# Optimization experiments

Hardware: AMD Instinct MI355X
Metric: run time of the kernel (lower is better)

Reference implementation:

```python
import jax, jax.numpy as jnp
import numpy as np

GMAX = 1.0   # args.gmax
GMIN = 0.01  # args.gmin
EPS = 0.1    # args.e_train


def setup_inputs() -> dict:
    key = jax.random.key(0)
    k1, k2, k3, k4 = jax.random.split(key, 4)
    N, B, NIN, NOUT, E = 8, 32, 128, 128, 1024
    # analog signals live in [0, 1]
    a_previous = jax.random.uniform(k1, (N, B, NIN, E), dtype=jnp.float32)
    # conductance params (clamped to [-gmax, gmax] in forward)
    theta = jax.random.uniform(k2, (NIN + 2, NOUT), dtype=jnp.float32) * 2.0 - 1.0
    # per-replica multiplicative noise seed in [0, 1); forward maps to 1 +- eps
    noise = jax.random.uniform(k3, (N, NIN + 2, NOUT), dtype=jnp.float32)
    # printed-tanh activation params eta = [offset, scale, shift, slope]
    eta = jnp.array([0.0, 1.0, 0.0, 1.0], dtype=jnp.float32) + 0.1 * jax.random.normal(k4, (4,), dtype=jnp.float32)
    return {"a_previous": a_previous, "theta": theta, "noise": noise, "eta": eta}


def reference(a_previous, theta, noise, eta):
    sg = jax.lax.stop_gradient
    # theta property: clamp + gmin pruning with straight-through estimator
    t = jnp.clip(theta, -GMAX, GMAX)
    t = jnp.where(jnp.abs(t) < GMIN, 0.0, t)
    theta_eff = sg(t) + theta - sg(theta)
    # theta_noisy: replicate over N with multiplicative uniform noise in [1-eps, 1+eps]
    theta_noisy = theta_eff[None, :, :] * ((noise * 2.0 - 1.0) * EPS + 1.0)  # [N, M, O], M = n_in+2
    # W: abs-normalized conductances per output column group
    abs_tn = jnp.abs(theta_noisy)
    W = abs_tn / (jnp.sum(abs_tn, axis=1, keepdims=True) + 1e-10)
    # sign masks (constants w.r.t. grad: values fully overwritten in torch)
    pos = sg((theta_noisy >= 0.0).astype(theta_noisy.dtype))
    neg = 1.0 - pos
    # a: [N, B, n_in, E] -> [N, B, E, n_in]; append ones and zeros columns
    a_r = jnp.transpose(a_previous, (0, 1, 3, 2))
    ones = jnp.ones(a_r.shape[:3] + (1,), a_r.dtype)
    zeros = jnp.zeros_like(ones)
    a_ext = jnp.concatenate([a_r, ones, zeros], axis=3)  # [N, B, E, M]
    # INV: unipolar complement; zero the last (zeros) column after inversion
    a_neg = (1.0 - a_ext).at[..., -1].set(0.0)
    # split-sign MAC: z [N, B, E, n_out]
    z = (jnp.einsum('nbem,nmo->nbeo', a_ext, W * pos)
         + jnp.einsum('nbem,nmo->nbeo', a_neg, W * neg))
    # printed tanh activation
    act = eta[0] + eta[1] * jnp.tanh((z - eta[2]) * eta[3])
    # back to [N, B, n_out, E]
    return jnp.transpose(act, (0, 1, 3, 2))
```

## Files before the change

### kernel.cpp

```cpp
#include <hip/hip_runtime.h>
#include <hip/hip_bf16.h>
#include <stdint.h>

#define N_REP 8
#define BATCH 32
#define NIN   128
#define NOUT  128
#define EDIM  1024
#define MDIM  130

typedef __attribute__((ext_vector_type(8))) short short8;
typedef __attribute__((ext_vector_type(4))) float f32x4;

__device__ __forceinline__ unsigned short f2bf(float f) {
    union { float f; uint32_t u; } v;
    v.f = f;
    uint32_t u = v.u;
    uint32_t r = u + 0x7fffu + ((u >> 16) & 1u);
    return (unsigned short)(r >> 16);
}

__device__ __forceinline__ uint32_t pk2bf(float lo, float hi) {
    __hip_bfloat162 h = __float22bfloat162_rn(make_float2(lo, hi));
    uint32_t d;
    __builtin_memcpy(&d, &h, 4);
    return d;
}

__global__ __launch_bounds__(64)
void prep_kernel(const float* __restrict__ theta,
                 const float* __restrict__ noise,
                 unsigned short* __restrict__ Sg,
                 float* __restrict__ biasg) {
    const int n = blockIdx.x >> 7;
    const int o = blockIdx.x & 127;
    const int lane = threadIdx.x;

    const float* nb = noise + (size_t)n * MDIM * NOUT + o;
    auto tn_at = [&](int m) -> float {
        float t = theta[m * NOUT + o];
        t = fminf(fmaxf(t, -1.f), 1.f);
        if (fabsf(t) < 0.01f) t = 0.f;
        return t * fmaf(nb[m * NOUT], 0.2f, 0.9f);
    };

    const float t0 = tn_at(lane);
    const float t1 = tn_at(lane + 64);
    const float t2 = (lane < 2) ? tn_at(128 + lane) : 0.f;

    float s = fabsf(t0) + fabsf(t1) + fabsf(t2);
#pragma unroll
    for (int d = 1; d < 64; d <<= 1) s += __shfl_xor(s, d, 64);
    const float inv = 1.f / (s + 1e-10f);

    const float w0 = fabsf(t0) * inv, w1 = fabsf(t1) * inv;
    unsigned short* srow = Sg + ((size_t)n * NOUT + o) * NIN;
    srow[lane]      = f2bf(t0 >= 0.f ? w0 : -w0);
    srow[lane + 64] = f2bf(t1 >= 0.f ? w1 : -w1);

    float b = (t0 < 0.f ? w0 : 0.f) + (t1 < 0.f ? w1 : 0.f);
    if (lane == 0 && t2 >= 0.f) b += fabsf(t2) * inv;
#pragma unroll
    for (int d = 1; d < 64; d <<= 1) b += __shfl_xor(b, d, 64);
    if (lane == 0) biasg[n * NOUT + o] = b;
}

__global__ __launch_bounds__(256, 3)
void gemm_kernel(const float* __restrict__ a,
                 const unsigned short* __restrict__ Sg,
                 const float* __restrict__ biasg,
                 const float* __restrict__ eta,
                 float* __restrict__ out) {
    const int bid  = blockIdx.x;
    const int tid  = threadIdx.x;
    const int lane = tid & 63;
    const int wv   = tid >> 6;
    const int r    = lane & 15;
    const int q    = lane >> 4;
    const int nb   = bid >> 3;
    const int n    = nb >> 5;
    const int e0w  = (((bid & 7) << 2) | wv) << 5;

    const float* abase = a + (size_t)nb * (NIN * EDIM) + e0w + r;

    float e0 = eta[0], e1 = eta[1], e2 = eta[2], e3 = eta[3];
    asm volatile("" : "+v"(e0), "+v"(e1), "+v"(e2), "+v"(e3));

    float bl[8];
#pragma unroll
    for (int fo = 0; fo < 8; ++fo)
        bl[fo] = biasg[n * NOUT + (fo << 4) + r];

    f32x4 acc[8][2];
#pragma unroll
    for (int fo = 0; fo < 8; ++fo)
#pragma unroll
        for (int fe = 0; fe < 2; ++fe)
            acc[fo][fe] = (f32x4){0.f, 0.f, 0.f, 0.f};

    const unsigned short* sbase = Sg + ((size_t)(n * NOUT) << 7) + (q << 3);

#pragma unroll
    for (int ks = 0; ks < 4; ++ks) {
        float av[2][8];
#pragma unroll
        for (int fe = 0; fe < 2; ++fe)
#pragma unroll
            for (int j = 0; j < 8; ++j)
                av[fe][j] = abase[(size_t)((ks << 5) + (q << 3) + j) * EDIM + (fe << 4)];

        short8 sf[8];
#pragma unroll
        for (int fo = 0; fo < 8; ++fo)
            sf[fo] = *(const short8*)(sbase + ((size_t)((fo << 4) + r) << 7) + (ks << 5));

        short8 af[2];
#pragma unroll
        for (int fe = 0; fe < 2; ++fe) {
            uint32_t d[4];
#pragma unroll
            for (int t = 0; t < 4; ++t)
                d[t] = pk2bf(av[fe][2 * t], av[fe][2 * t + 1]);
            __builtin_memcpy(&af[fe], d, 16);
        }

#pragma unroll
        for (int fo = 0; fo < 8; ++fo)
#pragma unroll
            for (int fe = 0; fe < 2; ++fe)
                acc[fo][fe] = __builtin_amdgcn_mfma_f32_16x16x32_bf16(
                    af[fe], sf[fo], acc[fo][fe], 0, 0, 0);
    }

    float* obase = out + (size_t)nb * (NOUT * EDIM) + e0w;
#pragma unroll
    for (int fo = 0; fo < 8; ++fo) {
        float* orow = obase + (size_t)((fo << 4) + r) * EDIM;
        const float bv = bl[fo];
#pragma unroll
        for (int fe = 0; fe < 2; ++fe) {
            f32x4 res;
#pragma unroll
            for (int i = 0; i < 4; ++i) {
                const float z = acc[fo][fe][i] + bv;
                const float y = (z - e2) * e3;
                const float ex = __expf(2.f * y);
                const float th = 1.f - 2.f * __builtin_amdgcn_rcpf(ex + 1.f);
                res[i] = fmaf(e1, th, e0);
            }
            *(f32x4*)(orow + (fe << 4) + (q << 2)) = res;
        }
    }
}

extern "C" void kernel_launch(void* const* d_in, const int* in_sizes, int n_in,
                              void* d_out, int out_size, void* d_ws, size_t ws_size,
                              hipStream_t stream) {
    const float* a     = (const float*)d_in[0];
    const float* theta = (const float*)d_in[1];
    const float* noise = (const float*)d_in[2];
    const float* eta   = (const float*)d_in[3];
    float* out = (float*)d_out;

    unsigned short* Sg = (unsigned short*)d_ws;
    float* biasg = (float*)((char*)d_ws + (size_t)N_REP * NOUT * NIN * sizeof(unsigned short));

    prep_kernel<<<N_REP * NOUT, 64, 0, stream>>>(theta, noise, Sg, biasg);
    gemm_kernel<<<N_REP * BATCH * 8, 256, 0, stream>>>(a, Sg, biasg, eta, out);
}
```

Baseline: 268.6 us.

## Stage A tiles through LDS with float4 loads and register prefetch

Activation loads switch from scalar per-lane global reads to float4 vector loads. The values are packed into bf16 pairs along k and written to a per-wave, padded, double-buffered LDS slice, from which the MFMA A-fragments are read. The next k-slice is prefetched into registers while MFMAs run on the current one, and weight fragments are loaded closer to their use. This aims to cut the number of global memory instructions and overlap load latency with compute, at the cost of LDS traffic and extra registers.

```diff
diff --git a/kernel.cpp b/kernel.cpp
--- a/kernel.cpp
+++ b/kernel.cpp
@@ -8,6 +8,8 @@
 #define NOUT  128
 #define EDIM  1024
 #define MDIM  130
+#define SROW  36
+#define SLICE (16 * SROW)
 
 typedef __attribute__((ext_vector_type(8))) short short8;
 typedef __attribute__((ext_vector_type(4))) float f32x4;
@@ -71,25 +73,46 @@
                  const float* __restrict__ biasg,
                  const float* __restrict__ eta,
                  float* __restrict__ out) {
+    __shared__ uint32_t Alds[4][2][SLICE];
     const int bid  = blockIdx.x;
+    const int nb   = bid >> 3;
+    const int n    = nb >> 5;
+    const int eb   = bid & 7;
     const int tid  = threadIdx.x;
     const int lane = tid & 63;
     const int wv   = tid >> 6;
     const int r    = lane & 15;
     const int q    = lane >> 4;
-    const int nb   = bid >> 3;
-    const int n    = nb >> 5;
-    const int e0w  = (((bid & 7) << 2) | wv) << 5;
+    const int e0   = (eb << 7) + (wv << 5);
 
-    const float* abase = a + (size_t)nb * (NIN * EDIM) + e0w + r;
+    const int mp_l = lane >> 2;
+    const int ec   = (lane & 3) << 2;
+    const float* abase = a + (size_t)nb * (NIN * EDIM) + e0 + ec;
+    uint32_t* L = &Alds[wv][0][0];
 
-    float e0 = eta[0], e1 = eta[1], e2 = eta[2], e3 = eta[3];
-    asm volatile("" : "+v"(e0), "+v"(e1), "+v"(e2), "+v"(e3));
+    float4 va[2], vb[2];
+    auto issue = [&](int t) {
+        const float* gp = abase + (size_t)(2 * mp_l + (t << 5)) * EDIM;
+#pragma unroll
+        for (int i = 0; i < 2; ++i) {
+            va[i] = *(const float4*)(gp + (i << 4));
+            vb[i] = *(const float4*)(gp + EDIM + (i << 4));
+        }
+    };
+    auto pack_write = [&](int buf) {
+#pragma unroll
+        for (int i = 0; i < 2; ++i) {
+            uint4 d;
+            d.x = pk2bf(va[i].x, vb[i].x);
+            d.y = pk2bf(va[i].y, vb[i].y);
+            d.z = pk2bf(va[i].z, vb[i].z);
+            d.w = pk2bf(va[i].w, vb[i].w);
+            *(uint4*)&L[buf * SLICE + mp_l * SROW + ec + (i << 4)] = d;
+        }
+    };
 
-    float bl[8];
-#pragma unroll
-    for (int fo = 0; fo < 8; ++fo)
-        bl[fo] = biasg[n * NOUT + (fo << 4) + r];
+    float e0f = eta[0], e1f = eta[1], e2f = eta[2], e3f = eta[3];
+    asm volatile("" : "+v"(e0f), "+v"(e1f), "+v"(e2f), "+v"(e3f));
 
     f32x4 acc[8][2];
 #pragma unroll
@@ -100,53 +123,55 @@
 
     const unsigned short* sbase = Sg + ((size_t)(n * NOUT) << 7) + (q << 3);
 
+    issue(0);
+    pack_write(0);
+    issue(1);
+
 #pragma unroll
-    for (int ks = 0; ks < 4; ++ks) {
-        float av[2][8];
-#pragma unroll
-        for (int fe = 0; fe < 2; ++fe)
-#pragma unroll
-            for (int j = 0; j < 8; ++j)
-                av[fe][j] = abase[(size_t)((ks << 5) + (q << 3) + j) * EDIM + (fe << 4)];
-
-        short8 sf[8];
-#pragma unroll
-        for (int fo = 0; fo < 8; ++fo)
-            sf[fo] = *(const short8*)(sbase + ((size_t)((fo << 4) + r) << 7) + (ks << 5));
-
+    for (int t = 0; t < 4; ++t) {
+        const int buf = t & 1;
         short8 af[2];
 #pragma unroll
         for (int fe = 0; fe < 2; ++fe) {
             uint32_t d[4];
 #pragma unroll
-            for (int t = 0; t < 4; ++t)
-                d[t] = pk2bf(av[fe][2 * t], av[fe][2 * t + 1]);
+            for (int jj = 0; jj < 4; ++jj)
+                d[jj] = L[buf * SLICE + ((q << 2) + jj) * SROW + (fe << 4) + r];
             __builtin_memcpy(&af[fe], d, 16);
         }
-
 #pragma unroll
-        for (int fo = 0; fo < 8; ++fo)
+        for (int fo2 = 0; fo2 < 4; ++fo2) {
+            const short8 s0 = *(const short8*)(sbase + ((size_t)((fo2 << 5) + r) << 7) + (t << 5));
+            const short8 s1 = *(const short8*)(sbase + ((size_t)((fo2 << 5) + 16 + r) << 7) + (t << 5));
 #pragma unroll
-            for (int fe = 0; fe < 2; ++fe)
-                acc[fo][fe] = __builtin_amdgcn_mfma_f32_16x16x32_bf16(
-                    af[fe], sf[fo], acc[fo][fe], 0, 0, 0);
+            for (int fe = 0; fe < 2; ++fe) {
+                acc[fo2 * 2][fe] = __builtin_amdgcn_mfma_f32_16x16x32_bf16(
+                    af[fe], s0, acc[fo2 * 2][fe], 0, 0, 0);
+                acc[fo2 * 2 + 1][fe] = __builtin_amdgcn_mfma_f32_16x16x32_bf16(
+                    af[fe], s1, acc[fo2 * 2 + 1][fe], 0, 0, 0);
+            }
+        }
+        if (t < 3) {
+            pack_write(buf ^ 1);
+            if (t < 2) issue(t + 2);
+        }
     }
 
-    float* obase = out + (size_t)nb * (NOUT * EDIM) + e0w;
+    float* obase = out + (size_t)nb * (NOUT * EDIM) + e0;
 #pragma unroll
     for (int fo = 0; fo < 8; ++fo) {
+        const float bv = biasg[n * NOUT + (fo << 4) + r];
         float* orow = obase + (size_t)((fo << 4) + r) * EDIM;
-        const float bv = bl[fo];
 #pragma unroll
         for (int fe = 0; fe < 2; ++fe) {
             f32x4 res;
 #pragma unroll
             for (int i = 0; i < 4; ++i) {
                 const float z = acc[fo][fe][i] + bv;
-                const float y = (z - e2) * e3;
+                const float y = (z - e2f) * e3f;
                 const float ex = __expf(2.f * y);
                 const float th = 1.f - 2.f * __builtin_amdgcn_rcpf(ex + 1.f);
-                res[i] = fmaf(e1, th, e0);
+                res[i] = fmaf(e1f, th, e0f);
             }
             *(f32x4*)(orow + (fe << 4) + (q << 2)) = res;
         }
```

Measured after the change: 270.2 us. No clear change (+0.6%).
